# Optimization experiments

Measured on AMD Instinct MI355X. Metric: run time of the kernel, lower is better.

The kernel has to match this reference:

```python
import jax, jax.numpy as jnp
import numpy as np

N_EMBD = 2048
DIM_ATT = 2048
HEAD_SIZE = 64
N_HEAD = DIM_ATT // HEAD_SIZE
D_MIX = 32
D_DECAY = 64
N_LAYER = 24
LAYER_ID = 12
EPS = 1e-5 * 8.0 ** 2  # GroupNorm eps with head_size_divisor=8


def setup_inputs() -> dict:
    key = jax.random.key(0)
    ks = jax.random.split(key, 10)
    B, T, C = 4, 2048, N_EMBD
    r0 = LAYER_ID / (N_LAYER - 1)          # ratio_0_to_1
    r1 = 1.0 - LAYER_ID / N_LAYER          # ratio_1_to_almost0
    ddd = (np.arange(C, dtype=np.float64) / C)
    f32 = np.float32
    time_maa_x = (1.0 - ddd ** r1).astype(f32)[None, None, :]
    time_maa_w = (1.0 - ddd ** r1).astype(f32)[None, None, :]
    time_maa_k = (1.0 - ddd ** r1).astype(f32)[None, None, :]
    time_maa_v = (1.0 - (ddd ** r1 + 0.3 * r0)).astype(f32)[None, None, :]
    time_maa_r = (1.0 - ddd ** (0.5 * r1)).astype(f32)[None, None, :]
    time_maa_g = (1.0 - ddd ** (0.5 * r1)).astype(f32)[None, None, :]
    n = np.arange(DIM_ATT, dtype=np.float64)
    decay_speed = (-6.0 + 5.0 * (n / (DIM_ATT - 1)) ** (0.7 + 1.3 * r0)).astype(f32)
    time_decay = decay_speed[None, None, :]
    zig = ((n + 1) % 3 - 1) * 0.1
    time_faaaa = (r0 * (1.0 - n / (DIM_ATT - 1)) + zig).astype(f32).reshape(N_HEAD, HEAD_SIZE)
    u = lambda k, sh: jax.random.uniform(k, sh, jnp.float32, -0.01, 0.01)
    inp = {
        'x': jax.random.normal(ks[0], (B, T, C), jnp.float32),
        'time_maa_x': jnp.asarray(time_maa_x), 'time_maa_w': jnp.asarray(time_maa_w),
        'time_maa_k': jnp.asarray(time_maa_k), 'time_maa_v': jnp.asarray(time_maa_v),
        'time_maa_r': jnp.asarray(time_maa_r), 'time_maa_g': jnp.asarray(time_maa_g),
        'time_maa_w1': u(ks[1], (C, D_MIX * 5)),
        'time_maa_w2': u(ks[2], (5, D_MIX, C)),
        'time_decay': jnp.asarray(time_decay),
        'time_decay_w1': u(ks[3], (C, D_DECAY)),
        'time_decay_w2': u(ks[4], (D_DECAY, DIM_ATT)),
        'time_faaaa': jnp.asarray(time_faaaa),
        'W_r': jax.random.normal(ks[5], (DIM_ATT, C), jnp.float32) * 0.02,
        'W_k': jax.random.normal(ks[6], (DIM_ATT, C), jnp.float32) * 0.02,
        'W_v': jax.random.normal(ks[7], (DIM_ATT, C), jnp.float32) * 0.02,
        'W_g': jax.random.normal(ks[8], (DIM_ATT, C), jnp.float32) * 0.02,
        'W_o': jax.random.normal(ks[9], (C, DIM_ATT), jnp.float32) * 0.02,
        'ln_gamma': jnp.ones((DIM_ATT,), jnp.float32),
        'ln_beta': jnp.zeros((DIM_ATT,), jnp.float32),
    }
    return inp


def _wkv6(r, k, v, w, u):
    # r,k,v,w: (B,T,H,N); u: (H,N). decay = exp(-exp(w)) applied per key-dim j.
    B, T, H, N = r.shape
    decay = jnp.exp(-jnp.exp(w))

    def step(S, inp):  # S: (B,H,N,N) indexed [b,h,j,i]
        r_t, k_t, v_t, d_t = inp  # each (B,H,N)
        kv = k_t[..., :, None] * v_t[..., None, :]          # (B,H,N,N)
        y = jnp.einsum('bhj,bhji->bhi', r_t, S + u[None, :, :, None] * kv)
        return d_t[..., None] * S + kv, y

    seq = (r.transpose(1, 0, 2, 3), k.transpose(1, 0, 2, 3),
           v.transpose(1, 0, 2, 3), decay.transpose(1, 0, 2, 3))
    S0 = jnp.zeros((B, H, N, N), r.dtype)
    _, ys = jax.lax.scan(step, S0, seq)                      # (T,B,H,N)
    return ys.transpose(1, 0, 2, 3)                          # (B,T,H,N)


def reference(x, time_maa_x, time_maa_w, time_maa_k, time_maa_v, time_maa_r, time_maa_g,
              time_maa_w1, time_maa_w2, time_decay, time_decay_w1, time_decay_w2,
              time_faaaa, W_r, W_k, W_v, W_g, W_o, ln_gamma, ln_beta):
    B, T, C = x.shape
    H, N = time_faaaa.shape
    xx = jnp.concatenate([jnp.zeros_like(x[:, :1]), x[:, :-1]], axis=1) - x  # time_shift - x
    xxx = x + xx * time_maa_x
    D = time_maa_w2.shape[1]
    a = jnp.tanh(xxx @ time_maa_w1).reshape(B, T, 5, D)
    m = jnp.einsum('btfd,fdc->fbtc', a, time_maa_w2)
    mw, mk, mv, mr, mg = m[0], m[1], m[2], m[3], m[4]
    xw = x + xx * (time_maa_w + mw)
    xk = x + xx * (time_maa_k + mk)
    xv = x + xx * (time_maa_v + mv)
    xr = x + xx * (time_maa_r + mr)
    xg = x + xx * (time_maa_g + mg)
    r = xr @ W_r.T
    k = xk @ W_k.T
    v = xv @ W_v.T
    g = jax.nn.silu(xg @ W_g.T)
    w = time_decay + jnp.tanh(xw @ time_decay_w1) @ time_decay_w2
    y = _wkv6(r.reshape(B, T, H, N), k.reshape(B, T, H, N),
              v.reshape(B, T, H, N), w.reshape(B, T, H, N), time_faaaa)
    # GroupNorm with H groups over channel dim
    mean = y.mean(-1, keepdims=True)
    var = y.var(-1, keepdims=True)
    yn = ((y - mean) * jax.lax.rsqrt(var + EPS)).reshape(B, T, H * N)
    yn = yn * ln_gamma + ln_beta
    return (yn * g) @ W_o.T
```

## Files before the change

kernel.cpp:

```cpp
#include <hip/hip_runtime.h>
#include <hip/hip_bf16.h>
#include <math.h>

#define B_ 4
#define T_ 2048
#define C_ 2048
#define H_ 32
#define BT_ 8192
#define WELE 4194304L
#define BTC  16777216L
#define NCH_ 16
#define TC_  128
#define GNT  32

typedef unsigned short u16;
typedef __bf16 bf16x8 __attribute__((ext_vector_type(8)));
typedef float  f32x4  __attribute__((ext_vector_type(4)));

__device__ __forceinline__ u16 f2b(float f){
  __hip_bfloat16 h = __float2bfloat16(f);
  return *reinterpret_cast<u16*>(&h);
}
__device__ __forceinline__ float b2f(u16 u){
  __hip_bfloat16 h; *reinterpret_cast<u16*>(&h) = u;
  return __bfloat162float(h);
}
__device__ __forceinline__ float bits2f(unsigned u){
  union { unsigned u; float f; } c; c.u = u; return c.f;
}

__device__ __forceinline__ void async_copy16(const u16* gptr, u16* lptr){
  __builtin_amdgcn_global_load_lds(
      (const __attribute__((address_space(1))) unsigned int*)gptr,
      (__attribute__((address_space(3))) unsigned int*)lptr,
      16, 0, 0);
}

__device__ __forceinline__ void unpack4(const u16* __restrict__ gp, float* out){
  const uint2 raw = *(const uint2*)gp;
  out[0] = bits2f(raw.x << 16); out[1] = bits2f(raw.x & 0xffff0000u);
  out[2] = bits2f(raw.y << 16); out[3] = bits2f(raw.y & 0xffff0000u);
}

__global__ __launch_bounds__(256) void cvt1(const float* __restrict__ src,
                                            u16* __restrict__ dst)
{
  const long i = ((long)blockIdx.x*256 + threadIdx.x)*4;
  const float4 v = *(const float4*)(src + i);
  ushort4 o = { f2b(v.x), f2b(v.y), f2b(v.z), f2b(v.w) };
  *(ushort4*)(dst + i) = o;
}

__global__ __launch_bounds__(256) void tposeA(const float* __restrict__ src,
    u16* __restrict__ dst, int R, int Cc, int Npad)
{
  const long idx = (long)blockIdx.x*256 + threadIdx.x;
  if (idx >= (long)Npad * R) return;
  const int n = (int)(idx / R), rr = (int)(idx % R);
  float vv = (n < Cc) ? src[(long)rr * Cc + n] : 0.f;
  dst[idx] = f2b(vv);
}

__global__ __launch_bounds__(256) void tposeW2(const float* __restrict__ src,
                                               u16* __restrict__ dst)
{
  const long idx = (long)blockIdx.x*256 + threadIdx.x;
  const int f = (int)(idx / 65536);
  const int rem = (int)(idx % 65536);
  const int c = rem >> 5, d = rem & 31;
  dst[idx] = f2b(src[((long)f*32 + d)*2048 + c]);
}

__global__ __launch_bounds__(256) void mixA(const float* __restrict__ x,
    const float* __restrict__ maax, u16* __restrict__ xxx, u16* __restrict__ xxb,
    u16* __restrict__ xbf)
{
  const long i = ((long)blockIdx.x*256 + threadIdx.x) * 4;
  const int c   = (int)(i & (C_-1));
  const int tok = (int)(i >> 11);
  const int t   = tok & (T_-1);
  const float4 xc = *(const float4*)(x + i);
  float4 xp = make_float4(0.f,0.f,0.f,0.f);
  if (t > 0) xp = *(const float4*)(x + i - C_);
  const float4 mx = *(const float4*)(maax + c);
  const float xx0 = xp.x - xc.x, xx1 = xp.y - xc.y;
  const float xx2 = xp.z - xc.z, xx3 = xp.w - xc.w;
  ushort4 ox = { f2b(xx0), f2b(xx1), f2b(xx2), f2b(xx3) };
  ushort4 o3 = { f2b(fmaf(xx0, mx.x, xc.x)), f2b(fmaf(xx1, mx.y, xc.y)),
                 f2b(fmaf(xx2, mx.z, xc.z)), f2b(fmaf(xx3, mx.w, xc.w)) };
  ushort4 oxb = { f2b(xc.x), f2b(xc.y), f2b(xc.z), f2b(xc.w) };
  *(ushort4*)(xxb + i) = ox;
  *(ushort4*)(xxx + i) = o3;
  *(ushort4*)(xbf + i) = oxb;
}

enum { EPI_BF16=0, EPI_TANH=1, EPI_SILU=2, EPI_MIX=3, EPI_DECAY=4, EPI_F32=5 };

template<int EPI>
__global__ __launch_bounds__(256) void gemm_bt(
    const u16* __restrict__ A, int lda,
    const u16* __restrict__ Bm, int ldb, int K,
    void* __restrict__ Out, int ldo,
    const float* __restrict__ aux0, const u16* __restrict__ aux1,
    const float* __restrict__ aux2)
{
  __shared__ u16 As[128*32];
  __shared__ u16 Bs[128*32];
  const int tid = threadIdx.x;
  const int w = tid >> 6, lane = tid & 63;
  const int m0 = blockIdx.y * 128, n0 = blockIdx.x * 128;
  const int wm = w >> 1, wn = w & 1;
  const int rowA = lane >> 2, chunk = lane & 3;
  f32x4 acc[4][4];
  #pragma unroll
  for (int i=0;i<4;i++)
    #pragma unroll
    for (int j=0;j<4;j++) acc[i][j] = (f32x4){0.f,0.f,0.f,0.f};

  for (int k0 = 0; k0 < K; k0 += 32){
    #pragma unroll
    for (int s=0; s<2; s++){
      const int seg = w*2 + s;
      const int row = seg*16 + rowA;
      async_copy16(A  + (long)(m0+row)*lda + k0 + chunk*8, As + seg*512);
      async_copy16(Bm + (long)(n0+row)*ldb + k0 + chunk*8, Bs + seg*512);
    }
    __syncthreads();
    const int kq = (lane >> 4) * 8;
    const int lr16 = lane & 15;
    bf16x8 af[4], bfr[4];
    #pragma unroll
    for (int mt=0; mt<4; mt++)
      af[mt] = *(const bf16x8*)(As + (wm*64 + mt*16 + lr16)*32 + kq);
    #pragma unroll
    for (int nt=0; nt<4; nt++)
      bfr[nt] = *(const bf16x8*)(Bs + (wn*64 + nt*16 + lr16)*32 + kq);
    #pragma unroll
    for (int mt=0; mt<4; mt++)
      #pragma unroll
      for (int nt=0; nt<4; nt++)
        acc[mt][nt] = __builtin_amdgcn_mfma_f32_16x16x32_bf16(af[mt], bfr[nt], acc[mt][nt], 0, 0, 0);
    __syncthreads();
  }

  const int cr = lane & 15, cq = lane >> 4;
  #pragma unroll
  for (int mt=0; mt<4; mt++){
    #pragma unroll
    for (int nt=0; nt<4; nt++){
      #pragma unroll
      for (int rr=0; rr<4; rr++){
        const int row = m0 + wm*64 + mt*16 + cq*4 + rr;
        const int col = n0 + wn*64 + nt*16 + cr;
        const long oi = (long)row*ldo + col;
        const float val = acc[mt][nt][rr];
        if constexpr (EPI == EPI_F32){
          ((float*)Out)[oi] = val;
        } else if constexpr (EPI == EPI_BF16){
          ((u16*)Out)[oi] = f2b(val);
        } else if constexpr (EPI == EPI_TANH){
          ((u16*)Out)[oi] = f2b(tanhf(val));
        } else if constexpr (EPI == EPI_SILU){
          ((u16*)Out)[oi] = f2b(val / (1.f + expf(-val)));
        } else if constexpr (EPI == EPI_MIX){
          const float xv  = b2f(((const u16*)aux0)[oi]);
          const float xxv = b2f(aux1[oi]);
          ((u16*)Out)[oi] = f2b(fmaf(xxv, aux2[col] + val, xv));
        } else {
          ((float*)Out)[oi] = expf(-expf(val + aux0[col]));
        }
      }
    }
  }
}

template<int EPI>
__global__ __launch_bounds__(512) void gemm256(
    const u16* __restrict__ A, const u16* __restrict__ Bm,
    void* __restrict__ Out, int ldo)
{
  __shared__ u16 lds[65536];
  const int tid  = threadIdx.x;
  const int w    = tid >> 6, lane = tid & 63;
  const int wm   = w >> 2, wn = w & 3;
  const long m0  = (long)blockIdx.y * 256;
  const long n0  = (long)blockIdx.x * 256;

  auto stage_half = [&](u16* ldsbase, const u16* gb){
    const int rsub = lane >> 3;
    const int c16  = (lane & 7) ^ rsub;
    #pragma unroll
    for (int r2 = 0; r2 < 2; ++r2){
      const int row = (r2*8 + w)*8 + rsub;
      async_copy16(gb + (long)row*2048 + c16*8,
                   ldsbase + (r2*8 + w)*512);
    }
  };
  auto stage = [&](int t, int half){
    if (t >= GNT) return;
    const int b = t & 1;
    const long k0 = (long)t * 64;
    if      (half == 0) stage_half(lds + 32768 + b*16384,        Bm + n0*2048 + k0);
    else if (half == 1) stage_half(lds + 32768 + b*16384 + 8192, Bm + (n0+128)*2048 + k0);
    else if (half == 2) stage_half(lds + b*16384,                A  + m0*2048 + k0);
    else                stage_half(lds + b*16384 + 8192,         A  + (m0+128)*2048 + k0);
  };

  const int lr16 = lane & 15;
  const int kq   = lane >> 4;
  auto aslot = [&](int buf, int row, int c16)->const u16*{
    return lds + buf*16384 + row*64 + ((c16 ^ (row & 7)) << 3);
  };
  auto bslot = [&](int buf, int row, int c16)->const u16*{
    return lds + 32768 + buf*16384 + row*64 + ((c16 ^ (row & 7)) << 3);
  };

  f32x4 acc[8][4];
  #pragma unroll
  for (int i=0;i<8;i++)
    #pragma unroll
    for (int j=0;j<4;j++) acc[i][j] = (f32x4){0.f,0.f,0.f,0.f};

  stage(0,0); stage(0,1); stage(0,2); stage(0,3);
  stage(1,0); stage(1,1); stage(1,2);
  asm volatile("s_waitcnt vmcnt(6)");
  asm volatile("" ::: "memory");
  __builtin_amdgcn_s_barrier();

  for (int t = 0; t < GNT; ++t){
    const int buf = t & 1;
    bf16x8 bfr[4][2];
    #pragma unroll
    for (int p = 0; p < 4; ++p){
      if (p == 0){
        #pragma unroll
        for (int nt=0; nt<4; nt++)
          #pragma unroll
          for (int kk=0; kk<2; kk++)
            bfr[nt][kk] = *(const bf16x8*)bslot(buf, wn*64 + nt*16 + lr16, kk*4 + kq);
      }
      bf16x8 af[2][2];
      #pragma unroll
      for (int i=0; i<2; i++)
        #pragma unroll
        for (int kk=0; kk<2; kk++)
          af[i][kk] = *(const bf16x8*)aslot(buf, wm*128 + (2*p+i)*16 + lr16, kk*4 + kq);
      if (p == 0) stage(t+1, 3);
      else        stage(t+2, p-1);
      if (p == 3){
        if (t <= GNT-3) asm volatile("s_waitcnt vmcnt(6)");
        else            asm volatile("s_waitcnt vmcnt(0)");
      }
      asm volatile("" ::: "memory");
      __builtin_amdgcn_s_barrier();
      __builtin_amdgcn_s_setprio(1);
      #pragma unroll
      for (int i=0; i<2; i++)
        #pragma unroll
        for (int nt=0; nt<4; nt++)
          #pragma unroll
          for (int kk=0; kk<2; kk++)
            acc[2*p+i][nt] = __builtin_amdgcn_mfma_f32_16x16x32_bf16(
                af[i][kk], bfr[nt][kk], acc[2*p+i][nt], 0, 0, 0);
      __builtin_amdgcn_s_setprio(0);
    }
  }

  const int cr = lane & 15, cq = lane >> 4;
  #pragma unroll
  for (int mt=0; mt<8; mt++){
    #pragma unroll
    for (int nt=0; nt<4; nt++){
      #pragma unroll
      for (int rr=0; rr<4; rr++){
        const long row = m0 + wm*128 + mt*16 + cq*4 + rr;
        const long col = n0 + wn*64 + nt*16 + cr;
        const long oi  = row*ldo + col;
        const float val = acc[mt][nt][rr];
        if constexpr (EPI == EPI_F32){
          ((float*)Out)[oi] = val;
        } else if constexpr (EPI == EPI_BF16){
          ((u16*)Out)[oi] = f2b(val);
        } else {
          ((u16*)Out)[oi] = f2b(val / (1.f + expf(-val)));
        }
      }
    }
  }
}

__global__ __launch_bounds__(256) void wkv_pass1(
    const u16* __restrict__ k, const u16* __restrict__ v,
    const float* __restrict__ dec,
    float* __restrict__ Sbuf, float* __restrict__ Dbuf)
{
  const int blk = blockIdx.x;
  const int c  = blk & (NCH_-1);
  if (c == NCH_-1) return;
  const int bh = blk >> 4;
  const int b = bh >> 5, h = bh & 31;
  const int tid = threadIdx.x;
  const int g = tid >> 6, lane = tid & 63;
  const int hoff = h * 64;
  const long base0 = ((long)b * T_) * C_ + hoff;
  const int tA = c * TC_;

  __shared__ float kts[128][64];
  __shared__ u16   vsh[128][64];
  __shared__ float Gp[4][64];

  #pragma unroll
  for (int rd = 0; rd < 4; ++rd){
    const int row0 = (rd*4 + g) * 8;
    async_copy16(v + base0 + (long)(tA + row0 + (lane>>3))*C_ + (lane&7)*8,
                 &vsh[row0][0]);
  }

  float d[32];
  float gp = 1.f;
  #pragma unroll
  for (int tau = 0; tau < 32; ++tau){
    d[tau] = dec[base0 + (long)(tA + g*32 + tau)*C_ + lane];
    gp *= d[tau];
  }
  Gp[g][lane] = gp;
  __syncthreads();
  float CS = 1.f;
  #pragma unroll
  for (int gg = 0; gg < 4; ++gg)
    if (gg > g) CS *= Gp[gg][lane];
  if (g == 0){
    Dbuf[(long)blk*64 + lane] =
        Gp[0][lane]*Gp[1][lane]*Gp[2][lane]*Gp[3][lane];
  }
  {
    float R = CS;
    #pragma unroll
    for (int tau = 31; tau >= 0; --tau){
      const float kv = b2f(k[base0 + (long)(tA + g*32 + tau)*C_ + lane]);
      kts[g*32 + tau][lane] = kv * R;
      R *= d[tau];
    }
  }
  __syncthreads();

  const int joff = g * 16;
  float S[16];
  #pragma unroll
  for (int jj=0;jj<16;jj++) S[jj]=0.f;
  #pragma unroll 4
  for (int t = 0; t < TC_; ++t){
    float kv[16];
    #pragma unroll
    for (int q=0;q<4;q++)
      *(float4*)(kv+q*4) = *(const float4*)&kts[t][joff+q*4];
    const float vi = b2f(vsh[t][lane]);
    #pragma unroll
    for (int jj=0;jj<16;jj++)
      S[jj] = fmaf(kv[jj], vi, S[jj]);
  }
  float* Sp = Sbuf + (long)blk*4096 + (long)joff*64 + lane;
  #pragma unroll
  for (int jj=0;jj<16;jj++) Sp[jj*64] = S[jj];
}

__global__ __launch_bounds__(256) void wkv_pass2(
    float* __restrict__ Sbuf, const float* __restrict__ Dbuf)
{
  const int bh = blockIdx.x >> 4;
  const int f  = ((blockIdx.x & 15) << 8) + threadIdx.x;
  const int j = f >> 6;
  float cur = 0.f;
  const long sbase = (long)bh * NCH_ * 4096 + f;
  const long dbase = (long)bh * NCH_ * 64 + j;
  for (int c = 0; c < NCH_-1; c++){
    float* Sp = Sbuf + sbase + (long)c*4096;
    const float tmp = *Sp;
    *Sp = cur;
    cur = fmaf(Dbuf[dbase + (long)c*64], cur, tmp);
  }
  Sbuf[sbase + (long)(NCH_-1)*4096] = cur;
}

__global__ __launch_bounds__(256) void wkv_pass3(
    const u16* __restrict__ r, const u16* __restrict__ k, const u16* __restrict__ v,
    const float* __restrict__ dec, const float* __restrict__ faaaa,
    const float* __restrict__ gam, const float* __restrict__ bet,
    const u16* __restrict__ g, u16* __restrict__ act,
    const float* __restrict__ Sbuf)
{
  const int blk = blockIdx.x;
  const int c  = blk & (NCH_-1);
  const int bh = blk >> 4;
  const int b = bh >> 5, h = bh & 31;
  const int tid = threadIdx.x;
  const int jg = tid >> 6, lane = tid & 63;
  const int hoff = h * 64;
  const int joff = jg * 16;

  float S[16];
  {
    const float* Sp = Sbuf + (long)blk*4096 + (long)joff*64 + lane;
    #pragma unroll
    for (int jj=0;jj<16;jj++) S[jj] = Sp[jj*64];
  }
  float u[16];
  #pragma unroll
  for (int jj=0;jj<16;jj++) u[jj] = faaaa[hoff + jg*16 + jj];
  const float gmv = gam[hoff + lane], btv = bet[hoff + lane];

  __shared__ float rs[16][64], ks[16][64], dsh[16][64], vs[16][64];
  __shared__ float yred[16][4][64];

  const long base0 = ((long)b * T_) * C_ + hoff;
  const int stt = tid >> 4;
  const int scc = (tid & 15) * 4;
  const int tA = c * TC_;

  for (int t0 = tA; t0 < tA + TC_; t0 += 16){
    __syncthreads();
    {
      const long gi = base0 + (long)(t0 + stt) * C_ + scc;
      float tmp[4];
      unpack4(r + gi, tmp);  *(float4*)&rs[stt][scc]  = *(float4*)tmp;
      unpack4(k + gi, tmp);  *(float4*)&ks[stt][scc]  = *(float4*)tmp;
      unpack4(v + gi, tmp);  *(float4*)&vs[stt][scc]  = *(float4*)tmp;
      *(float4*)&dsh[stt][scc] = *(const float4*)(dec + gi);
    }
    __syncthreads();
    #pragma unroll 2
    for (int tt = 0; tt < 16; tt++){
      float rv[16], kv[16], dv[16];
      #pragma unroll
      for (int q=0;q<4;q++){
        *(float4*)(rv+q*4) = *(const float4*)&rs[tt][joff+q*4];
        *(float4*)(kv+q*4) = *(const float4*)&ks[tt][joff+q*4];
        *(float4*)(dv+q*4) = *(const float4*)&dsh[tt][joff+q*4];
      }
      const float vi = vs[tt][lane];
      float yp = 0.f;
      #pragma unroll
      for (int jj=0;jj<16;jj++){
        const float p = kv[jj] * vi;
        yp = fmaf(rv[jj], fmaf(u[jj], p, S[jj]), yp);
        S[jj] = fmaf(dv[jj], S[jj], p);
      }
      yred[tt][jg][lane] = yp;
    }
    __syncthreads();
    #pragma unroll
    for (int q=0;q<4;q++){
      const int tt = jg*4 + q;
      const float y = yred[tt][0][lane] + yred[tt][1][lane]
                    + yred[tt][2][lane] + yred[tt][3][lane];
      float s1 = y, s2 = y*y;
      #pragma unroll
      for (int off=32; off>0; off>>=1){
        s1 += __shfl_xor(s1, off, 64);
        s2 += __shfl_xor(s2, off, 64);
      }
      const float mean = s1 * (1.f/64.f);
      const float var  = s2 * (1.f/64.f) - mean*mean;
      const float yn   = (y - mean) * rsqrtf(var + 6.4e-4f);
      const long  oi   = base0 + (long)(t0 + tt) * C_ + lane;
      const float o    = (yn * gmv + btv) * b2f(g[oi]);
      act[oi] = f2b(o);
    }
  }
}

extern "C" void kernel_launch(void* const* d_in, const int* in_sizes, int n_in,
                              void* d_out, int out_size, void* d_ws, size_t ws_size,
                              hipStream_t stream)
{
  const float* x     = (const float*)d_in[0];
  const float* tmx   = (const float*)d_in[1];
  const float* maaf[5] = {(const float*)d_in[2], (const float*)d_in[3],
                          (const float*)d_in[4], (const float*)d_in[5],
                          (const float*)d_in[6]};
  const float* w1    = (const float*)d_in[7];
  const float* w2    = (const float*)d_in[8];
  const float* td    = (const float*)d_in[9];
  const float* tdw1  = (const float*)d_in[10];
  const float* tdw2  = (const float*)d_in[11];
  const float* faaaa = (const float*)d_in[12];
  const float* Wmat[5] = {(const float*)d_in[13], (const float*)d_in[14],
                          (const float*)d_in[15], (const float*)d_in[16],
                          (const float*)d_in[17]};
  const float* ln_g  = (const float*)d_in[18];
  const float* ln_b  = (const float*)d_in[19];

  char* p = (char*)d_ws;
  auto take = [&](size_t bytes)->char*{
    char* q = p; p += (bytes + 255) & ~(size_t)255; return q;
  };
  u16*   w1t  = (u16*)take(256L*2048*2);
  u16*   w2t  = (u16*)take(5L*2048*32*2);
  u16*   wd1t = (u16*)take(128L*2048*2);
  u16*   wd2t = (u16*)take(2048L*64*2);
  u16*   wcur = (u16*)take(WELE*2);
  u16*   xxx  = (u16*)take(BTC*2);
  u16*   xxb  = (u16*)take(BTC*2);
  u16*   abuf = (u16*)take((long)BT_*256*2);
  u16*   hbuf = (u16*)take((long)BT_*128*2);
  u16*   kbuf = (u16*)take(BTC*2);
  u16*   vbuf = (u16*)take(BTC*2);
  u16*   gbuf = (u16*)take(BTC*2);
  u16*   mixbuf = xxx;
  u16*   rbuf   = xxb;
  u16*   act    = kbuf;
  float* dcy    = (float*)d_out;
  u16*   xbf    = (u16*)d_out;
  float* Sbuf   = (float*)mixbuf;
  float* Dbuf   = (float*)hbuf;
  (void)in_sizes; (void)n_in; (void)out_size; (void)ws_size;

  tposeA <<<2048, 256, 0, stream>>>(w1,   w1t,  2048, 160, 256);
  tposeW2<<<1280, 256, 0, stream>>>(w2,   w2t);
  tposeA <<<1024, 256, 0, stream>>>(tdw1, wd1t, 2048, 64, 128);
  tposeA <<<512,  256, 0, stream>>>(tdw2, wd2t, 64, 2048, 2048);

  mixA<<<16384, 256, 0, stream>>>(x, tmx, xxx, xxb, xbf);

  gemm_bt<EPI_TANH><<<dim3(2,64), 256, 0, stream>>>(xxx, 2048, w1t, 2048, 2048,
      abuf, 256, nullptr, nullptr, nullptr);


  gemm_bt<EPI_MIX><<<dim3(16,64), 256, 0, stream>>>(abuf + 1*32, 256,
      w2t + 1L*65536, 32, 32, mixbuf, 2048, (const float*)xbf, xxb, maaf[1]);
  cvt1<<<4096, 256, 0, stream>>>(Wmat[1], wcur);
  gemm256<EPI_BF16><<<dim3(8,32), 512, 0, stream>>>(mixbuf, wcur, kbuf, 2048);

  gemm_bt<EPI_MIX><<<dim3(16,64), 256, 0, stream>>>(abuf + 2*32, 256,
      w2t + 2L*65536, 32, 32, mixbuf, 2048, (const float*)xbf, xxb, maaf[2]);
  cvt1<<<4096, 256, 0, stream>>>(Wmat[2], wcur);
  gemm256<EPI_BF16><<<dim3(8,32), 512, 0, stream>>>(mixbuf, wcur, vbuf, 2048);

  gemm_bt<EPI_MIX><<<dim3(16,64), 256, 0, stream>>>(abuf + 4*32, 256,
      w2t + 4L*65536, 32, 32, mixbuf, 2048, (const float*)xbf, xxb, maaf[4]);
  cvt1<<<4096, 256, 0, stream>>>(Wmat[3], wcur);
  gemm256<EPI_SILU><<<dim3(8,32), 512, 0, stream>>>(mixbuf, wcur, gbuf, 2048);

  gemm_bt<EPI_MIX><<<dim3(16,64), 256, 0, stream>>>(abuf + 0*32, 256,
      w2t + 0L*65536, 32, 32, mixbuf, 2048, (const float*)xbf, xxb, maaf[0]);
  gemm_bt<EPI_TANH><<<dim3(1,64), 256, 0, stream>>>(mixbuf, 2048, wd1t, 2048, 2048,
      hbuf, 128, nullptr, nullptr, nullptr);

  gemm_bt<EPI_MIX><<<dim3(16,64), 256, 0, stream>>>(abuf + 3*32, 256,
      w2t + 3L*65536, 32, 32, mixbuf, 2048, (const float*)xbf, xxb, maaf[3]);
  cvt1<<<4096, 256, 0, stream>>>(Wmat[0], wcur);
  gemm256<EPI_BF16><<<dim3(8,32), 512, 0, stream>>>(mixbuf, wcur, rbuf, 2048);

  gemm_bt<EPI_DECAY><<<dim3(16,64), 256, 0, stream>>>(hbuf, 128, wd2t, 64, 64,
      dcy, 2048, td, nullptr, nullptr);

  wkv_pass1<<<128*NCH_, 256, 0, stream>>>(kbuf, vbuf, dcy, Sbuf, Dbuf);
  wkv_pass2<<<128*NCH_, 256, 0, stream>>>(Sbuf, Dbuf);
  wkv_pass3<<<128*NCH_, 256, 0, stream>>>(rbuf, kbuf, vbuf, dcy, faaaa,
      ln_g, ln_b, gbuf, act, Sbuf);

  cvt1<<<4096, 256, 0, stream>>>(Wmat[4], wcur);
  gemm256<EPI_F32><<<dim3(8,32), 512, 0, stream>>>(act, wcur, d_out, 2048);
}
```

Measured before the change: 1.009 ms.

## Reformulate WKV pass3 with cumulative-decay rescaled r/k to drop per-step decay

Rewrites the chunk-local WKV output kernel so that within each 32-step subchunk r is prescaled by the cumulative decay and k divided by it. The state update becomes a pure rank-1 add and the state is rescaled once per subchunk. The bonus term u*k*v is computed separately through a per-timestep wave reduction. This removes the per-step decay multiply and the separate decay tile from the inner loop, at the cost of extra setup work and possible numerical trouble from dividing by small cumulative decay products.

```diff
diff --git a/kernel.cpp b/kernel.cpp
--- a/kernel.cpp
+++ b/kernel.cpp
@@ -289,6 +289,7 @@
   }
 }
 
+
 __global__ __launch_bounds__(256) void wkv_pass1(
     const u16* __restrict__ k, const u16* __restrict__ v,
     const float* __restrict__ dec,
@@ -394,78 +395,113 @@
   const int bh = blk >> 4;
   const int b = bh >> 5, h = bh & 31;
   const int tid = threadIdx.x;
-  const int jg = tid >> 6, lane = tid & 63;
+  const int wv = tid >> 6, lane = tid & 63;
   const int hoff = h * 64;
-  const int joff = jg * 16;
-
-  float S[16];
+  const int joff = wv * 16;
+
+  float W[16];
   {
     const float* Sp = Sbuf + (long)blk*4096 + (long)joff*64 + lane;
     #pragma unroll
-    for (int jj=0;jj<16;jj++) S[jj] = Sp[jj*64];
-  }
-  float u[16];
-  #pragma unroll
-  for (int jj=0;jj<16;jj++) u[jj] = faaaa[hoff + jg*16 + jj];
+    for (int jj=0;jj<16;jj++) W[jj] = Sp[jj*64];
+  }
+  const float uu  = faaaa[hoff + lane];
   const float gmv = gam[hoff + lane], btv = bet[hoff + lane];
 
-  __shared__ float rs[16][64], ks[16][64], dsh[16][64], vs[16][64];
+  __shared__ float rhat[32][64];
+  __shared__ float ktil[32][64];
+  __shared__ u16   vsh[32][64];
   __shared__ float yred[16][4][64];
+  __shared__ float Gp[4][64];
+  __shared__ float cendL[64];
+  __shared__ float ud[32];
 
   const long base0 = ((long)b * T_) * C_ + hoff;
-  const int stt = tid >> 4;
-  const int scc = (tid & 15) * 4;
   const int tA = c * TC_;
 
-  for (int t0 = tA; t0 < tA + TC_; t0 += 16){
+  for (int sc = 0; sc < TC_/32; ++sc){
+    const int t0 = tA + sc*32;
     __syncthreads();
+    async_copy16(v + base0 + (long)(t0 + wv*8 + (lane>>3))*C_ + (lane&7)*8,
+                 &vsh[wv*8][0]);
+    float dloc[8];
+    float gp = 1.f;
+    #pragma unroll
+    for (int tau=0; tau<8; ++tau){
+      dloc[tau] = dec[base0 + (long)(t0 + wv*8 + tau)*C_ + lane];
+      gp *= dloc[tau];
+    }
+    Gp[wv][lane] = gp;
+    __syncthreads();
+    float cpre = 1.f;
+    #pragma unroll
+    for (int gg=0; gg<4; ++gg) if (gg < wv) cpre *= Gp[gg][lane];
+    if (wv == 0)
+      cendL[lane] = Gp[0][lane]*Gp[1][lane]*Gp[2][lane]*Gp[3][lane];
     {
-      const long gi = base0 + (long)(t0 + stt) * C_ + scc;
-      float tmp[4];
-      unpack4(r + gi, tmp);  *(float4*)&rs[stt][scc]  = *(float4*)tmp;
-      unpack4(k + gi, tmp);  *(float4*)&ks[stt][scc]  = *(float4*)tmp;
-      unpack4(v + gi, tmp);  *(float4*)&vs[stt][scc]  = *(float4*)tmp;
-      *(float4*)&dsh[stt][scc] = *(const float4*)(dec + gi);
+      float cc = cpre;
+      #pragma unroll
+      for (int tau=0; tau<8; ++tau){
+        const int tl = wv*8 + tau;
+        const long gi = base0 + (long)(t0 + tl)*C_ + lane;
+        const float rv = b2f(r[gi]);
+        const float kv = b2f(k[gi]);
+        rhat[tl][lane] = rv * cc;
+        float z = rv * uu * kv;
+        cc *= dloc[tau];
+        ktil[tl][lane] = kv / cc;
+        #pragma unroll
+        for (int off=32; off>0; off>>=1) z += __shfl_xor(z, off, 64);
+        if (lane == 0) ud[tl] = z;
+      }
     }
     __syncthreads();
-    #pragma unroll 2
-    for (int tt = 0; tt < 16; tt++){
-      float rv[16], kv[16], dv[16];
+
+    #pragma unroll
+    for (int half=0; half<2; ++half){
+      #pragma unroll 2
+      for (int tt=0; tt<16; ++tt){
+        const int tl = half*16 + tt;
+        float rv[16], kt[16];
+        #pragma unroll
+        for (int q=0;q<4;q++){
+          *(float4*)(rv+q*4) = *(const float4*)&rhat[tl][joff+q*4];
+          *(float4*)(kt+q*4) = *(const float4*)&ktil[tl][joff+q*4];
+        }
+        const float vi = b2f(vsh[tl][lane]);
+        float yp = 0.f;
+        #pragma unroll
+        for (int jj=0;jj<16;jj++){
+          yp = fmaf(rv[jj], W[jj], yp);
+          W[jj] = fmaf(kt[jj], vi, W[jj]);
+        }
+        yred[tt][wv][lane] = yp;
+      }
+      __syncthreads();
       #pragma unroll
       for (int q=0;q<4;q++){
-        *(float4*)(rv+q*4) = *(const float4*)&rs[tt][joff+q*4];
-        *(float4*)(kv+q*4) = *(const float4*)&ks[tt][joff+q*4];
-        *(float4*)(dv+q*4) = *(const float4*)&dsh[tt][joff+q*4];
-      }
-      const float vi = vs[tt][lane];
-      float yp = 0.f;
-      #pragma unroll
-      for (int jj=0;jj<16;jj++){
-        const float p = kv[jj] * vi;
-        yp = fmaf(rv[jj], fmaf(u[jj], p, S[jj]), yp);
-        S[jj] = fmaf(dv[jj], S[jj], p);
-      }
-      yred[tt][jg][lane] = yp;
-    }
-    __syncthreads();
-    #pragma unroll
-    for (int q=0;q<4;q++){
-      const int tt = jg*4 + q;
-      const float y = yred[tt][0][lane] + yred[tt][1][lane]
-                    + yred[tt][2][lane] + yred[tt][3][lane];
-      float s1 = y, s2 = y*y;
-      #pragma unroll
-      for (int off=32; off>0; off>>=1){
-        s1 += __shfl_xor(s1, off, 64);
-        s2 += __shfl_xor(s2, off, 64);
-      }
-      const float mean = s1 * (1.f/64.f);
-      const float var  = s2 * (1.f/64.f) - mean*mean;
-      const float yn   = (y - mean) * rsqrtf(var + 6.4e-4f);
-      const long  oi   = base0 + (long)(t0 + tt) * C_ + lane;
-      const float o    = (yn * gmv + btv) * b2f(g[oi]);
-      act[oi] = f2b(o);
-    }
+        const int tt = wv*4 + q;
+        const int tl = half*16 + tt;
+        const float y = yred[tt][0][lane] + yred[tt][1][lane]
+                      + yred[tt][2][lane] + yred[tt][3][lane]
+                      + ud[tl] * b2f(vsh[tl][lane]);
+        float s1 = y, s2 = y*y;
+        #pragma unroll
+        for (int off=32; off>0; off>>=1){
+          s1 += __shfl_xor(s1, off, 64);
+          s2 += __shfl_xor(s2, off, 64);
+        }
+        const float mean = s1 * (1.f/64.f);
+        const float var  = s2 * (1.f/64.f) - mean*mean;
+        const float yn   = (y - mean) * rsqrtf(var + 6.4e-4f);
+        const long  oi   = base0 + (long)(t0 + tl) * C_ + lane;
+        const float o    = (yn * gmv + btv) * b2f(g[oi]);
+        act[oi] = f2b(o);
+      }
+      if (half == 0) __syncthreads();
+    }
+    #pragma unroll
+    for (int jj=0;jj<16;jj++) W[jj] *= cendL[joff + jj];
   }
 }
 
@@ -525,7 +561,6 @@
   gemm_bt<EPI_TANH><<<dim3(2,64), 256, 0, stream>>>(xxx, 2048, w1t, 2048, 2048,
       abuf, 256, nullptr, nullptr, nullptr);
 
-
   gemm_bt<EPI_MIX><<<dim3(16,64), 256, 0, stream>>>(abuf + 1*32, 256,
       w2t + 1L*65536, 32, 32, mixbuf, 2048, (const float*)xbf, xxb, maaf[1]);
   cvt1<<<4096, 256, 0, stream>>>(Wmat[1], wcur);
```

Measured after the change: 992.4 us (median of 2 runs). Within noise of the previous version (-1.6%).
